# Performance work log

Hardware: AMD Instinct MI355X
Metric: run time of the kernel (lower is better)

## Reference

```python
import jax, jax.numpy as jnp
import numpy as np

B, S, D_IN, D_OUT, L = 16, 1024, 768, 768, 2
ALPHA = 0.2  # LeakyReLU negative slope
NEG_INF = -1e12


def setup_inputs() -> dict:
    key = jax.random.key(0)
    ks = jax.random.split(key, 6)
    input_feature = jax.random.normal(ks[0], (B, S, D_IN), dtype=jnp.float32)
    matrix = jax.random.randint(ks[1], (B, S, S), 0, 2, dtype=jnp.int32)
    # per-layer params (stacked along leading L axis)
    sw = 1.0 / np.sqrt(D_IN)
    W = jax.random.uniform(ks[2], (L, D_OUT, D_IN), jnp.float32, -sw, sw)
    Wb = jax.random.uniform(ks[3], (L, D_OUT), jnp.float32, -sw, sw)
    sa = 1.0 / np.sqrt(2 * D_OUT)
    A = jax.random.uniform(ks[4], (L, 2 * D_OUT), jnp.float32, -sa, sa)
    Ab = jax.random.uniform(ks[5], (L,), jnp.float32, -sa, sa)
    return {"input_feature": input_feature, "matrix": matrix,
            "W": W, "Wb": Wb, "A": A, "Ab": Ab}


def reference(input_feature, matrix, W, Wb, A, Ab):
    # Eval mode: dropout(p=0.1, training=False) is identity.
    hidden = input_feature
    mask = matrix > 0  # [B,S,S]
    outs = []
    for l in range(L):
        h = jnp.einsum('bsd,od->bso', hidden, W[l]) + Wb[l]  # [B,S,Dout]
        # a([h_i, h_j]) == h_i @ a_src + h_j @ a_dst + b  (exact separation)
        a_src, a_dst = A[l, :D_OUT], A[l, D_OUT:]
        s_i = h @ a_src  # [B,S]
        s_j = h @ a_dst  # [B,S]
        e = jax.nn.leaky_relu(s_i[:, :, None] + s_j[:, None, :] + Ab[l], ALPHA)
        e = jnp.where(mask, e, NEG_INF)
        attn = jax.nn.softmax(e, axis=1)  # original softmaxes over dim=1
        hidden = jnp.einsum('bij,bjd->bid', attn, h)
        outs.append(hidden)
    return jnp.stack(outs)  # [L,B,S,Dout]
```

## Files before the change

kernel.cpp:

```cpp
#include <hip/hip_runtime.h>
#include <cstddef>

#define SS 1024
#define DF 768
#define NBATCH 16
#define GAT_ALPHA 0.2f

typedef _Float16 f16x8 __attribute__((ext_vector_type(8)));
typedef _Float16 f16x4 __attribute__((ext_vector_type(4)));
typedef float f32x4 __attribute__((ext_vector_type(4)));

__device__ __forceinline__ void gload16(const void* g, void* l) {
  __builtin_amdgcn_global_load_lds(
      (const __attribute__((address_space(1))) void*)g,
      (__attribute__((address_space(3))) void*)l, 16, 0, 0);
}

__device__ __forceinline__ float lrelu(float t) {
  return fmaxf(t, GAT_ALPHA * t);
}

__global__ __launch_bounds__(256) void f32tof16_k(const float* __restrict__ in,
                                                  _Float16* __restrict__ out,
                                                  int n) {
  int idx = (blockIdx.x * 256 + threadIdx.x) * 4;
  if (idx + 3 < n) {
    float4 v = *(const float4*)&in[idx];
    f16x4 o;
    o[0] = (_Float16)v.x;
    o[1] = (_Float16)v.y;
    o[2] = (_Float16)v.z;
    o[3] = (_Float16)v.w;
    *(f16x4*)&out[idx] = o;
  }
}

__global__ __launch_bounds__(256) void pack_k(const int* __restrict__ mask,
                                              unsigned char* __restrict__ bm) {
  const size_t t = (size_t)blockIdx.x * 256 + threadIdx.x;
  const int* mp = mask + t * 8;
  const int4 a = *(const int4*)mp;
  const int4 c = *(const int4*)(mp + 4);
  unsigned v = (unsigned)(a.x > 0) | ((unsigned)(a.y > 0) << 1) |
               ((unsigned)(a.z > 0) << 2) | ((unsigned)(a.w > 0) << 3) |
               ((unsigned)(c.x > 0) << 4) | ((unsigned)(c.y > 0) << 5) |
               ((unsigned)(c.z > 0) << 6) | ((unsigned)(c.w > 0) << 7);
  bm[t] = (unsigned char)v;
}


__global__ __launch_bounds__(512, 2) void gemm1_k(
    const _Float16* __restrict__ X16, const _Float16* __restrict__ W16,
    const float* __restrict__ Wbl, const float* __restrict__ Al,
    _Float16* __restrict__ hT16, float* __restrict__ psi2,
    float* __restrict__ psj2) {
  __shared__ __align__(16) char smem[131072];
  const int flat = blockIdx.x;
  const int swz = (flat & 7) * 32 + (flat >> 3);
  const int m0 = (swz >> 1) * 128;
  const int n0 = (swz & 1) * 384;
  const int tid = threadIdx.x;
  const int w = tid >> 6, lane = tid & 63;

  const int srow = w * 16 + (lane >> 2);
  const int sk8 = ((lane & 3) ^ ((lane >> 3) & 3)) * 8;
  const int rby = ((lane >> 4) ^ ((lane >> 1) & 3)) * 16;
  const int rrow = lane & 15;

  f32x4 acc[8][3];
#pragma unroll
  for (int mi = 0; mi < 8; ++mi)
#pragma unroll
    for (int ni = 0; ni < 3; ++ni) acc[mi][ni] = (f32x4)(0.f);

#define STGA1(s, kt)                                                       \
  gload16(&X16[(size_t)(m0 + srow) * DF + (kt) * 32 + sk8],                \
          smem + (s) * 32768 + w * 1024)
#define STGB1(s, kt, q)                                                    \
  gload16(&W16[(size_t)(n0 + (q) * 128 + srow) * DF + (kt) * 32 + sk8],    \
          smem + (s) * 32768 + 8192 + (q) * 8192 + w * 1024)

  const int NT = DF / 32;
  STGA1(0, 0); STGB1(0, 0, 0); STGB1(0, 0, 1); STGB1(0, 0, 2);
  STGA1(1, 1); STGB1(1, 1, 0); STGB1(1, 1, 1); STGB1(1, 1, 2);
  asm volatile("s_waitcnt vmcnt(4)" ::: "memory");
  asm volatile("s_barrier" ::: "memory");

  for (int t = 0; t < NT; ++t) {
    const int s = t & 3;
    const char* Ab = smem + s * 32768;
    const char* Bb = smem + s * 32768 + 8192;
    f16x8 bfr[3], afr[8];
#pragma unroll
    for (int ni = 0; ni < 3; ++ni)
      bfr[ni] = *(const f16x8*)(Bb + (w * 48 + ni * 16 + rrow) * 64 + rby);
#pragma unroll
    for (int mi = 0; mi < 8; ++mi)
      afr[mi] = *(const f16x8*)(Ab + (mi * 16 + rrow) * 64 + rby);
    if (t + 2 < NT) {
      const int s2 = (t + 2) & 3;
      STGA1(s2, t + 2);
      STGB1(s2, t + 2, 0);
      STGB1(s2, t + 2, 1);
      STGB1(s2, t + 2, 2);
    }
    if (t < NT - 2)
      asm volatile("s_waitcnt vmcnt(4)" ::: "memory");
    else
      asm volatile("s_waitcnt vmcnt(0)" ::: "memory");
    asm volatile("s_barrier" ::: "memory");
    __builtin_amdgcn_s_setprio(1);
#pragma unroll
    for (int mi = 0; mi < 8; ++mi)
#pragma unroll
      for (int ni = 0; ni < 3; ++ni)
        acc[mi][ni] = __builtin_amdgcn_mfma_f32_16x16x32_f16(
            afr[mi], bfr[ni], acc[mi][ni], 0, 0, 0);
    __builtin_amdgcn_s_setprio(0);
  }
#undef STGA1
#undef STGB1

  __syncthreads();

  _Float16* tb = (_Float16*)smem + (size_t)w * 6528;
  float* asrc = (float*)(smem + 104448);
  float* adst = asrc + 384;
  float* pwsi = adst + 384;
  float* pwsj = pwsi + 1024;

  for (int i = tid; i < 384; i += 512) {
    asrc[i] = Al[n0 + i];
    adst[i] = Al[DF + n0 + i];
  }
  const int cg = lane >> 4, cr = lane & 15;
  float bias[3];
#pragma unroll
  for (int ni = 0; ni < 3; ++ni) bias[ni] = Wbl[n0 + w * 48 + ni * 16 + cr];
#pragma unroll
  for (int mi = 0; mi < 8; ++mi) {
#pragma unroll
    for (int ni = 0; ni < 3; ++ni) {
      f16x4 tv;
#pragma unroll
      for (int r = 0; r < 4; ++r)
        tv[r] = (_Float16)(acc[mi][ni][r] + bias[ni]);
      *(f16x4*)&tb[(ni * 16 + cr) * 136 + mi * 16 + cg * 4] = tv;
    }
  }
  __syncthreads();

  const float* wa = asrc + w * 48;
  const float* wdp = adst + w * 48;
#pragma unroll
  for (int rr = 0; rr < 2; ++rr) {
    const int r = lane + rr * 64;
    float ps = 0.f, pd = 0.f;
#pragma unroll 8
    for (int c = 0; c < 48; ++c) {
      const float hv = (float)tb[c * 136 + r];
      ps = fmaf(hv, wa[c], ps);
      pd = fmaf(hv, wdp[c], pd);
    }
    pwsi[w * 128 + r] = ps;
    pwsj[w * 128 + r] = pd;
  }
  __syncthreads();
  if (tid < 128) {
    float s = 0.f, d2 = 0.f;
#pragma unroll
    for (int ww = 0; ww < 8; ++ww) {
      s += pwsi[ww * 128 + tid];
      d2 += pwsj[ww * 128 + tid];
    }
    const int nt = swz & 1;
    psi2[nt * 16384 + m0 + tid] = s;
    psj2[nt * 16384 + m0 + tid] = d2;
  }

  const int bb = m0 >> 10, s0 = m0 & 1023;
#pragma unroll
  for (int pass = 0; pass < 12; ++pass) {
    const int c = pass * 4 + (lane >> 4);
    f16x8 v = *(const f16x8*)&tb[c * 136 + (lane & 15) * 8];
    *(f16x8*)&hT16[((size_t)bb * DF + n0 + w * 48 + c) * SS + s0 +
                   (lane & 15) * 8] = v;
  }
}

__global__ __launch_bounds__(512, 2) void gemm2_k(
    const _Float16* __restrict__ P16, const _Float16* __restrict__ hT16,
    float* __restrict__ outl, _Float16* __restrict__ X16n, int writeX) {
  __shared__ __align__(16) char smem[131072];
  const int flat = blockIdx.x;
  const int swz = (flat & 7) * 32 + (flat >> 3);
  const int b = swz >> 4;
  const int i0 = ((swz >> 1) & 7) * 128;
  const int d0 = (swz & 1) * 384;
  const int tid = threadIdx.x;
  const int w = tid >> 6, lane = tid & 63;

  const int srow = w * 16 + (lane >> 2);
  const int sk8 = ((lane & 3) ^ ((lane >> 3) & 3)) * 8;
  const int rby = ((lane >> 4) ^ ((lane >> 1) & 3)) * 16;
  const int rrow = lane & 15;

  const _Float16* Pb = P16 + ((size_t)b << 20);
  const _Float16* hTb = hT16 + (size_t)b * DF * SS;

  f32x4 acc[8][3];
#pragma unroll
  for (int mi = 0; mi < 8; ++mi)
#pragma unroll
    for (int ni = 0; ni < 3; ++ni) acc[mi][ni] = (f32x4)(0.f);

#define STGA2(s, kt)                                                       \
  gload16(&Pb[((size_t)(i0 + srow) << 10) + (kt) * 32 + sk8],              \
          smem + (s) * 32768 + w * 1024)
#define STGB2(s, kt, q)                                                    \
  gload16(&hTb[((size_t)(d0 + (q) * 128 + srow)) * SS + (kt) * 32 + sk8],  \
          smem + (s) * 32768 + 8192 + (q) * 8192 + w * 1024)

  const int NT = SS / 32;
  STGA2(0, 0); STGB2(0, 0, 0); STGB2(0, 0, 1); STGB2(0, 0, 2);
  STGA2(1, 1); STGB2(1, 1, 0); STGB2(1, 1, 1); STGB2(1, 1, 2);
  asm volatile("s_waitcnt vmcnt(4)" ::: "memory");
  asm volatile("s_barrier" ::: "memory");

  for (int t = 0; t < NT; ++t) {
    const int s = t & 3;
    const char* Ab = smem + s * 32768;
    const char* Bb = smem + s * 32768 + 8192;
    f16x8 bfr[3], afr[8];
#pragma unroll
    for (int ni = 0; ni < 3; ++ni)
      bfr[ni] = *(const f16x8*)(Bb + (w * 48 + ni * 16 + rrow) * 64 + rby);
#pragma unroll
    for (int mi = 0; mi < 8; ++mi)
      afr[mi] = *(const f16x8*)(Ab + (mi * 16 + rrow) * 64 + rby);
    if (t + 2 < NT) {
      const int s2 = (t + 2) & 3;
      STGA2(s2, t + 2);
      STGB2(s2, t + 2, 0);
      STGB2(s2, t + 2, 1);
      STGB2(s2, t + 2, 2);
    }
    if (t < NT - 2)
      asm volatile("s_waitcnt vmcnt(4)" ::: "memory");
    else
      asm volatile("s_waitcnt vmcnt(0)" ::: "memory");
    asm volatile("s_barrier" ::: "memory");
    __builtin_amdgcn_s_setprio(1);
#pragma unroll
    for (int mi = 0; mi < 8; ++mi)
#pragma unroll
      for (int ni = 0; ni < 3; ++ni)
        acc[mi][ni] = __builtin_amdgcn_mfma_f32_16x16x32_f16(
            afr[mi], bfr[ni], acc[mi][ni], 0, 0, 0);
    __builtin_amdgcn_s_setprio(0);
  }
#undef STGA2
#undef STGB2

  const int cg = lane >> 4, cr = lane & 15;
#pragma unroll
  for (int mi = 0; mi < 8; ++mi) {
#pragma unroll
    for (int ni = 0; ni < 3; ++ni) {
      const int d = d0 + w * 48 + ni * 16 + cr;
      const int row0 = i0 + mi * 16 + cg * 4;
#pragma unroll
      for (int r = 0; r < 4; ++r) {
        float v = acc[mi][ni][r];
        size_t o = ((size_t)b * SS + row0 + r) * DF + d;
        outl[o] = v;
        if (writeX) X16n[o] = (_Float16)v;
      }
    }
  }
}

__global__ __launch_bounds__(256) void rowfin_k(const float* __restrict__ psi2,
                                                const float* __restrict__ psj2,
                                                const float* __restrict__ Abp,
                                                float* __restrict__ si,
                                                float* __restrict__ sjc,
                                                float* __restrict__ refj) {
  const int b = blockIdx.x;
  const int t = threadIdx.x;
  __shared__ float red[256];
  float siv[4], sjv[4];
  float mloc = -1e30f;
#pragma unroll
  for (int q = 0; q < 4; ++q) {
    const int idx = (b << 10) + t + (q << 8);
    const float a = psi2[idx] + psi2[16384 + idx];
    const float d = psj2[idx] + psj2[16384 + idx];
    siv[q] = a;
    sjv[q] = d;
    si[idx] = a;
    mloc = fmaxf(mloc, a);
  }
  red[t] = mloc;
  __syncthreads();
  for (int off = 128; off > 0; off >>= 1) {
    if (t < off) red[t] = fmaxf(red[t], red[t + off]);
    __syncthreads();
  }
  const float maxsi = red[0];
  const float ab = Abp[0];
#pragma unroll
  for (int q = 0; q < 4; ++q) {
    const int idx = (b << 10) + t + (q << 8);
    const float c = sjv[q] + ab;
    sjc[idx] = c;
    refj[idx] = lrelu(maxsi + c);
  }
}

__global__ __launch_bounds__(256) void colsum_k(
    const unsigned char* __restrict__ bm, const float* __restrict__ si,
    const float* __restrict__ sjc, const float* __restrict__ refj,
    float* __restrict__ pden) {
  const int g = blockIdx.x;
  const int b = blockIdx.y;
  const int t = threadIdx.x;
  const int jb = t & 127;
  const int half = t >> 7;
  const int row0 = (g << 5) + (half << 4);
  __shared__ float s_si[32];
  if (t < 32) s_si[t] = si[(b << 10) + (g << 5) + t];
  __syncthreads();
  float sc[8], rf[8];
  *(float4*)&sc[0] = *(const float4*)&sjc[(b << 10) + jb * 8];
  *(float4*)&sc[4] = *(const float4*)&sjc[(b << 10) + jb * 8 + 4];
  *(float4*)&rf[0] = *(const float4*)&refj[(b << 10) + jb * 8];
  *(float4*)&rf[4] = *(const float4*)&refj[(b << 10) + jb * 8 + 4];
  float den[8] = {0.f, 0.f, 0.f, 0.f, 0.f, 0.f, 0.f, 0.f};
  const unsigned char* bp = bm + ((size_t)b << 17) + ((size_t)row0 << 7) + jb;
#pragma unroll 4
  for (int r = 0; r < 16; ++r) {
    const unsigned m = bp[(size_t)r << 7];
    const float siv = s_si[(half << 4) + r];
#pragma unroll
    for (int k = 0; k < 8; ++k) {
      if ((m >> k) & 1) den[k] += __expf(lrelu(siv + sc[k]) - rf[k]);
    }
  }
  const size_t o = ((size_t)(g * 2 + half)) * 16384 + (b << 10) + jb * 8;
  *(float4*)&pden[o] = *(float4*)&den[0];
  *(float4*)&pden[o + 4] = *(float4*)&den[4];
}

__global__ __launch_bounds__(256) void colcomb_k(const float* __restrict__ pden,
                                                 float* __restrict__ rden) {
  const int idx = blockIdx.x * 256 + threadIdx.x;
  float s = 0.f;
#pragma unroll
  for (int c = 0; c < 64; ++c) s += pden[(size_t)c * 16384 + idx];
  rden[idx] = (s > 0.f) ? 1.f / s : -1.f;
}

__global__ __launch_bounds__(256) void punorm2_k(
    const unsigned char* __restrict__ bm, const float* __restrict__ si,
    const float* __restrict__ sjc, const float* __restrict__ refj,
    const float* __restrict__ rden, _Float16* __restrict__ P16) {
  const int g = blockIdx.x;
  const int b = blockIdx.y;
  const int t = threadIdx.x;
  const int jb = t & 127;
  const int half = t >> 7;
  const int row0 = (g << 5) + (half << 4);
  __shared__ float s_si[32];
  if (t < 32) s_si[t] = si[(b << 10) + (g << 5) + t];
  __syncthreads();
  float sc[8], rf[8], rd[8];
  *(float4*)&sc[0] = *(const float4*)&sjc[(b << 10) + jb * 8];
  *(float4*)&sc[4] = *(const float4*)&sjc[(b << 10) + jb * 8 + 4];
  *(float4*)&rf[0] = *(const float4*)&refj[(b << 10) + jb * 8];
  *(float4*)&rf[4] = *(const float4*)&refj[(b << 10) + jb * 8 + 4];
  *(float4*)&rd[0] = *(const float4*)&rden[(b << 10) + jb * 8];
  *(float4*)&rd[4] = *(const float4*)&rden[(b << 10) + jb * 8 + 4];
  const unsigned char* bp = bm + ((size_t)b << 17) + ((size_t)row0 << 7) + jb;
  _Float16* pp = P16 + ((size_t)b << 20) + ((size_t)row0 << 10) + jb * 8;
#pragma unroll 4
  for (int r = 0; r < 16; ++r) {
    const unsigned m = bp[(size_t)r << 7];
    const float siv = s_si[(half << 4) + r];
    f16x8 ph;
#pragma unroll
    for (int k = 0; k < 8; ++k) {
      float p;
      if (rd[k] < 0.f)
        p = 0.0009765625f;
      else if ((m >> k) & 1)
        p = __expf(lrelu(siv + sc[k]) - rf[k]) * rd[k];
      else
        p = 0.f;
      ph[k] = (_Float16)p;
    }
    *(f16x8*)(pp + ((size_t)r << 10)) = ph;
  }
}

extern "C" void kernel_launch(void* const* d_in, const int* in_sizes, int n_in,
                              void* d_out, int out_size, void* d_ws,
                              size_t ws_size, hipStream_t stream) {
  const float* X0 = (const float*)d_in[0];
  const int* mask = (const int*)d_in[1];
  const float* W = (const float*)d_in[2];
  const float* Wb = (const float*)d_in[3];
  const float* A = (const float*)d_in[4];
  const float* Ab = (const float*)d_in[5];
  float* out = (float*)d_out;

  const size_t BSD = (size_t)NBATCH * SS * DF;
  const size_t BSS = (size_t)NBATCH * SS * SS;
  const size_t BS = (size_t)NBATCH * SS;

  char* p = (char*)d_ws;
  _Float16* X16 = (_Float16*)p;   p += BSD * 2;
  _Float16* hT16 = (_Float16*)p;  p += BSD * 2;
  _Float16* P16 = (_Float16*)p;   p += BSS * 2;
  _Float16* W16 = (_Float16*)p;   p += (size_t)2 * DF * DF * 2;
  unsigned char* bmk = (unsigned char*)p; p += BSS / 8;
  float* psi2 = (float*)p; p += 2 * BS * 4;
  float* psj2 = (float*)p; p += 2 * BS * 4;
  float* pden = (float*)p; p += 64 * BS * 4;
  float* si = (float*)p;   p += BS * 4;
  float* sjc = (float*)p;  p += BS * 4;
  float* refj = (float*)p; p += BS * 4;
  float* rden = (float*)p; p += BS * 4;

  f32tof16_k<<<12288, 256, 0, stream>>>(X0, X16, (int)BSD);
  f32tof16_k<<<1152, 256, 0, stream>>>(W, W16, 2 * DF * DF);
  pack_k<<<8192, 256, 0, stream>>>(mask, bmk);

  for (int l = 0; l < 2; ++l) {
    gemm1_k<<<256, 512, 0, stream>>>(X16, W16 + (size_t)l * DF * DF,
                                     Wb + (size_t)l * DF,
                                     A + (size_t)l * 2 * DF, hT16, psi2, psj2);
    rowfin_k<<<16, 256, 0, stream>>>(psi2, psj2, Ab + l, si, sjc, refj);
    colsum_k<<<dim3(32, 16), 256, 0, stream>>>(bmk, si, sjc, refj, pden);
    colcomb_k<<<64, 256, 0, stream>>>(pden, rden);
    punorm2_k<<<dim3(32, 16), 256, 0, stream>>>(bmk, si, sjc, refj, rden, P16);
    gemm2_k<<<256, 512, 0, stream>>>(P16, hT16, out + (size_t)l * BSD, X16,
                                     (l == 0) ? 1 : 0);
  }
}
```

Measured before the change: 255.0 us.

## Fuse attention probability generation into the aggregation GEMM, dropping the P16 buffer

The separate punorm2 kernel, which wrote a dense fp16 attention matrix P to global memory, is removed. gemm2 now builds each P tile in shared memory from the packed mask bits, the per-row source score and a per-column packed (score, exp(-ref)/den) pair, overlapping that work with the MFMA pipeline. This avoids writing and re-reading a 32 MB P matrix per layer and one launch. In exchange it adds exp ALU work inside the GEMM, raises LDS use to 150 KB, and stores the column terms in fp16, which slightly changes precision.

Measured after the change: 246.2 us. -3.5%, faster.

```diff
diff --git a/kernel.cpp b/kernel.cpp
--- a/kernel.cpp
+++ b/kernel.cpp
@@ -48,7 +48,6 @@
   bm[t] = (unsigned char)v;
 }
 
-
 __global__ __launch_bounds__(512, 2) void gemm1_k(
     const _Float16* __restrict__ X16, const _Float16* __restrict__ W16,
     const float* __restrict__ Wbl, const float* __restrict__ Al,
@@ -122,7 +121,6 @@
 #undef STGB1
 
   __syncthreads();
-
   _Float16* tb = (_Float16*)smem + (size_t)w * 6528;
   float* asrc = (float*)(smem + 104448);
   float* adst = asrc + 384;
@@ -189,9 +187,10 @@
 }
 
 __global__ __launch_bounds__(512, 2) void gemm2_k(
-    const _Float16* __restrict__ P16, const _Float16* __restrict__ hT16,
+    const unsigned char* __restrict__ bmk, const float* __restrict__ si_g,
+    const unsigned int* __restrict__ sq_g, const _Float16* __restrict__ hT16,
     float* __restrict__ outl, _Float16* __restrict__ X16n, int writeX) {
-  __shared__ __align__(16) char smem[131072];
+  __shared__ __align__(16) char smem[153600];
   const int flat = blockIdx.x;
   const int swz = (flat & 7) * 32 + (flat >> 3);
   const int b = swz >> 4;
@@ -205,7 +204,9 @@
   const int rby = ((lane >> 4) ^ ((lane >> 1) & 3)) * 16;
   const int rrow = lane & 15;
 
-  const _Float16* Pb = P16 + ((size_t)b << 20);
+  const int pr = tid >> 2, pc = tid & 3;
+  const int ppos = pc ^ ((pr >> 1) & 3);
+
   const _Float16* hTb = hT16 + (size_t)b * DF * SS;
 
   f32x4 acc[8][3];
@@ -214,23 +215,60 @@
 #pragma unroll
     for (int ni = 0; ni < 3; ++ni) acc[mi][ni] = (f32x4)(0.f);
 
-#define STGA2(s, kt)                                                       \
-  gload16(&Pb[((size_t)(i0 + srow) << 10) + (kt) * 32 + sk8],              \
-          smem + (s) * 32768 + w * 1024)
 #define STGB2(s, kt, q)                                                    \
   gload16(&hTb[((size_t)(d0 + (q) * 128 + srow)) * SS + (kt) * 32 + sk8],  \
           smem + (s) * 32768 + 8192 + (q) * 8192 + w * 1024)
 
+#define COMPUTE_P(kt, slot)                                                  \
+  {                                                                          \
+    const unsigned mw =                                                      \
+        *(const unsigned*)(smem + 135168 + pr * 144 + (kt) * 4);             \
+    const unsigned mb = (mw >> (pc * 8)) & 0xffu;                            \
+    const f16x8 sA_ =                                                        \
+        *(const f16x8*)(smem + 131072 + (kt) * 128 + pc * 32);               \
+    const f16x8 sB_ =                                                        \
+        *(const f16x8*)(smem + 131072 + (kt) * 128 + pc * 32 + 16);          \
+    f16x8 ph;                                                                \
+    _Pragma("unroll") for (int jj = 0; jj < 4; ++jj) {                       \
+      const float sjcv = (float)sA_[2 * jj];                                 \
+      const float qv = (float)sA_[2 * jj + 1];                               \
+      const float ttv = siv + sjcv;                                          \
+      const float ev = __expf(fmaxf(ttv, 0.2f * ttv)) * qv;                  \
+      ph[jj] = (_Float16)(qv < 0.f ? -qv : (((mb >> jj) & 1u) ? ev : 0.f));  \
+    }                                                                        \
+    _Pragma("unroll") for (int jj = 0; jj < 4; ++jj) {                       \
+      const float sjcv = (float)sB_[2 * jj];                                 \
+      const float qv = (float)sB_[2 * jj + 1];                               \
+      const float ttv = siv + sjcv;                                          \
+      const float ev = __expf(fmaxf(ttv, 0.2f * ttv)) * qv;                  \
+      ph[4 + jj] = (_Float16)(qv < 0.f ? -qv                                 \
+                                       : (((mb >> (4 + jj)) & 1u) ? ev       \
+                                                                  : 0.f));   \
+    }                                                                        \
+    *(f16x8*)(smem + (slot) * 32768 + pr * 64 + ppos * 16) = ph;             \
+  }
+
+  const unsigned char* bmb = bmk + ((size_t)b << 17) + ((size_t)i0 << 7);
+  const uint4 mg0 = *(const uint4*)(bmb + tid * 32);
+  const uint4 mg1 = *(const uint4*)(bmb + tid * 32 + 16);
+  if (w < 4)
+    gload16(&sq_g[(b << 10) + w * 256 + lane * 4], smem + 131072 + w * 1024);
+  const float siv = si_g[(b << 10) + i0 + pr];
   const int NT = SS / 32;
-  STGA2(0, 0); STGB2(0, 0, 0); STGB2(0, 0, 1); STGB2(0, 0, 2);
-  STGA2(1, 1); STGB2(1, 1, 0); STGB2(1, 1, 1); STGB2(1, 1, 2);
-  asm volatile("s_waitcnt vmcnt(4)" ::: "memory");
+  STGB2(0, 0, 0); STGB2(0, 0, 1); STGB2(0, 0, 2);
+  STGB2(1, 1, 0); STGB2(1, 1, 1); STGB2(1, 1, 2);
+  asm volatile("s_waitcnt vmcnt(0)" ::: "memory");
+  *(uint4*)(smem + 135168 + pr * 144 + pc * 32) = mg0;
+  *(uint4*)(smem + 135168 + pr * 144 + pc * 32 + 16) = mg1;
+  asm volatile("s_waitcnt lgkmcnt(0)" ::: "memory");
   asm volatile("s_barrier" ::: "memory");
+  COMPUTE_P(0, 0);
+  asm volatile("s_waitcnt lgkmcnt(0)" ::: "memory");
+  asm volatile("s_barrier" ::: "memory");
 
   for (int t = 0; t < NT; ++t) {
-    const int s = t & 3;
-    const char* Ab = smem + s * 32768;
-    const char* Bb = smem + s * 32768 + 8192;
+    const char* Ab = smem + (t & 3) * 32768;
+    const char* Bb = Ab + 8192;
     f16x8 bfr[3], afr[8];
 #pragma unroll
     for (int ni = 0; ni < 3; ++ni)
@@ -238,17 +276,17 @@
 #pragma unroll
     for (int mi = 0; mi < 8; ++mi)
       afr[mi] = *(const f16x8*)(Ab + (mi * 16 + rrow) * 64 + rby);
+    if (t + 1 < NT) COMPUTE_P(t + 1, (t + 1) & 3);
     if (t + 2 < NT) {
       const int s2 = (t + 2) & 3;
-      STGA2(s2, t + 2);
       STGB2(s2, t + 2, 0);
       STGB2(s2, t + 2, 1);
       STGB2(s2, t + 2, 2);
     }
     if (t < NT - 2)
-      asm volatile("s_waitcnt vmcnt(4)" ::: "memory");
+      asm volatile("s_waitcnt vmcnt(3) lgkmcnt(0)" ::: "memory");
     else
-      asm volatile("s_waitcnt vmcnt(0)" ::: "memory");
+      asm volatile("s_waitcnt vmcnt(0) lgkmcnt(0)" ::: "memory");
     asm volatile("s_barrier" ::: "memory");
     __builtin_amdgcn_s_setprio(1);
 #pragma unroll
@@ -259,8 +297,8 @@
             afr[mi], bfr[ni], acc[mi][ni], 0, 0, 0);
     __builtin_amdgcn_s_setprio(0);
   }
-#undef STGA2
 #undef STGB2
+#undef COMPUTE_P
 
   const int cg = lane >> 4, cr = lane & 15;
 #pragma unroll
@@ -352,55 +390,21 @@
   *(float4*)&pden[o + 4] = *(float4*)&den[4];
 }
 
-__global__ __launch_bounds__(256) void colcomb_k(const float* __restrict__ pden,
-                                                 float* __restrict__ rden) {
+__global__ __launch_bounds__(256) void colfin_k(const float* __restrict__ pden,
+                                                const float* __restrict__ sjc,
+                                                const float* __restrict__ refj,
+                                                unsigned int* __restrict__ sq) {
   const int idx = blockIdx.x * 256 + threadIdx.x;
   float s = 0.f;
 #pragma unroll
   for (int c = 0; c < 64; ++c) s += pden[(size_t)c * 16384 + idx];
-  rden[idx] = (s > 0.f) ? 1.f / s : -1.f;
-}
-
-__global__ __launch_bounds__(256) void punorm2_k(
-    const unsigned char* __restrict__ bm, const float* __restrict__ si,
-    const float* __restrict__ sjc, const float* __restrict__ refj,
-    const float* __restrict__ rden, _Float16* __restrict__ P16) {
-  const int g = blockIdx.x;
-  const int b = blockIdx.y;
-  const int t = threadIdx.x;
-  const int jb = t & 127;
-  const int half = t >> 7;
-  const int row0 = (g << 5) + (half << 4);
-  __shared__ float s_si[32];
-  if (t < 32) s_si[t] = si[(b << 10) + (g << 5) + t];
-  __syncthreads();
-  float sc[8], rf[8], rd[8];
-  *(float4*)&sc[0] = *(const float4*)&sjc[(b << 10) + jb * 8];
-  *(float4*)&sc[4] = *(const float4*)&sjc[(b << 10) + jb * 8 + 4];
-  *(float4*)&rf[0] = *(const float4*)&refj[(b << 10) + jb * 8];
-  *(float4*)&rf[4] = *(const float4*)&refj[(b << 10) + jb * 8 + 4];
-  *(float4*)&rd[0] = *(const float4*)&rden[(b << 10) + jb * 8];
-  *(float4*)&rd[4] = *(const float4*)&rden[(b << 10) + jb * 8 + 4];
-  const unsigned char* bp = bm + ((size_t)b << 17) + ((size_t)row0 << 7) + jb;
-  _Float16* pp = P16 + ((size_t)b << 20) + ((size_t)row0 << 10) + jb * 8;
-#pragma unroll 4
-  for (int r = 0; r < 16; ++r) {
-    const unsigned m = bp[(size_t)r << 7];
-    const float siv = s_si[(half << 4) + r];
-    f16x8 ph;
-#pragma unroll
-    for (int k = 0; k < 8; ++k) {
-      float p;
-      if (rd[k] < 0.f)
-        p = 0.0009765625f;
-      else if ((m >> k) & 1)
-        p = __expf(lrelu(siv + sc[k]) - rf[k]) * rd[k];
-      else
-        p = 0.f;
-      ph[k] = (_Float16)p;
-    }
-    *(f16x8*)(pp + ((size_t)r << 10)) = ph;
-  }
+  const float q = (s > 0.f) ? __expf(-refj[idx]) / s : -0.0009765625f;
+  const _Float16 h0 = (_Float16)sjc[idx];
+  const _Float16 h1 = (_Float16)q;
+  unsigned short u0, u1;
+  __builtin_memcpy(&u0, &h0, 2);
+  __builtin_memcpy(&u1, &h1, 2);
+  sq[idx] = ((unsigned)u1 << 16) | (unsigned)u0;
 }
 
 extern "C" void kernel_launch(void* const* d_in, const int* in_sizes, int n_in,
@@ -421,7 +425,6 @@
   char* p = (char*)d_ws;
   _Float16* X16 = (_Float16*)p;   p += BSD * 2;
   _Float16* hT16 = (_Float16*)p;  p += BSD * 2;
-  _Float16* P16 = (_Float16*)p;   p += BSS * 2;
   _Float16* W16 = (_Float16*)p;   p += (size_t)2 * DF * DF * 2;
   unsigned char* bmk = (unsigned char*)p; p += BSS / 8;
   float* psi2 = (float*)p; p += 2 * BS * 4;
@@ -430,7 +433,7 @@
   float* si = (float*)p;   p += BS * 4;
   float* sjc = (float*)p;  p += BS * 4;
   float* refj = (float*)p; p += BS * 4;
-  float* rden = (float*)p; p += BS * 4;
+  unsigned int* sq_g = (unsigned int*)p; p += BS * 4;
 
   f32tof16_k<<<12288, 256, 0, stream>>>(X0, X16, (int)BSD);
   f32tof16_k<<<1152, 256, 0, stream>>>(W, W16, 2 * DF * DF);
@@ -442,9 +445,9 @@
                                      A + (size_t)l * 2 * DF, hT16, psi2, psj2);
     rowfin_k<<<16, 256, 0, stream>>>(psi2, psj2, Ab + l, si, sjc, refj);
     colsum_k<<<dim3(32, 16), 256, 0, stream>>>(bmk, si, sjc, refj, pden);
-    colcomb_k<<<64, 256, 0, stream>>>(pden, rden);
-    punorm2_k<<<dim3(32, 16), 256, 0, stream>>>(bmk, si, sjc, refj, rden, P16);
-    gemm2_k<<<256, 512, 0, stream>>>(P16, hT16, out + (size_t)l * BSD, X16,
+    colfin_k<<<64, 256, 0, stream>>>(pden, sjc, refj, sq_g);
+    gemm2_k<<<256, 512, 0, stream>>>(bmk, si, sq_g, hT16,
+                                     out + (size_t)l * BSD, X16,
                                      (l == 0) ? 1 : 0);
   }
 }
```
